# Performance work log

Hardware: AMD Instinct MI355X
Metric: run time of the kernel (lower is better)

The kernel has to match this reference:

```python
import jax, jax.numpy as jnp
import numpy as np
import math

N = 8192
NFEAT = 63
NHID = 1024
NLAYERS = 7
LAMBDA = 1.5
ALPHA = 0.7
NEG = -1e12


def setup_inputs() -> dict:
    key = jax.random.key(0)
    ks = jax.random.split(key, 12)
    x = jax.random.normal(ks[0], (N, NFEAT), dtype=jnp.float32)
    # dist acts as a (normalized) propagation matrix; scale by 1/N for numerical stability
    dist = jax.random.uniform(ks[1], (N, N), dtype=jnp.float32) / N
    adj = jax.random.randint(ks[2], (N, N), 0, 2, dtype=jnp.int32)
    # parameters
    fc_W = jax.random.normal(ks[3], (NFEAT, NHID), dtype=jnp.float32) * 0.1
    fc_b = jnp.zeros((NHID,), dtype=jnp.float32)
    stdv = 1.0 / math.sqrt(NHID)
    conv_W = jax.random.uniform(ks[4], (NLAYERS, NHID, NHID), dtype=jnp.float32,
                                minval=-stdv, maxval=stdv)
    gat_W = jax.random.normal(ks[5], (NHID, NHID), dtype=jnp.float32) * (1.414 / math.sqrt(NHID))
    gat_a = jax.random.normal(ks[6], (2 * NHID, 1), dtype=jnp.float32) * 0.05
    cls1_W = jax.random.normal(ks[7], (NHID, 64), dtype=jnp.float32) * (1.0 / math.sqrt(NHID))
    cls1_b = jnp.zeros((64,), dtype=jnp.float32)
    cls3_W = jax.random.normal(ks[8], (64, 1), dtype=jnp.float32) * 0.125
    cls3_b = jnp.zeros((1,), dtype=jnp.float32)
    return {"x": x, "dist": dist, "adj": adj, "fc_W": fc_W, "fc_b": fc_b,
            "conv_W": conv_W, "gat_W": gat_W, "gat_a": gat_a,
            "cls1_W": cls1_W, "cls1_b": cls1_b, "cls3_W": cls3_W, "cls3_b": cls3_b}


def _theta(l):
    return min(1.0, math.log(LAMBDA / l + 1.0))


def reference(x, dist, adj, fc_W, fc_b, conv_W, gat_W, gat_a, cls1_W, cls1_b, cls3_W, cls3_b):
    # eval mode: all dropouts are identity
    h = jax.nn.relu(x @ fc_W + fc_b)          # [N, H]
    h0 = h
    # GCNII-style propagation layers
    for i in range(NLAYERS):
        theta = _theta(i + 1)
        hi = dist @ h                          # [N, H] sparse-style propagation
        support = (1.0 - ALPHA) * hi + ALPHA * h0
        out = theta * (support @ conv_W[i]) + (1.0 - theta) * support + h
        h = jax.nn.relu(out)
    # GAT layer (l = 9). Faithful math, but computed without the N*N*2F tensor:
    # e_ij = leakyrelu(h_i' @ a1 + h_j' @ a2) with h' = h @ W
    hp = h @ gat_W                             # [N, H]
    a1 = gat_a[:NHID, 0]                       # [H]
    a2 = gat_a[NHID:, 0]                       # [H]
    e = jax.nn.leaky_relu(hp @ a1[:, None] + (hp @ a2[:, None]).T, negative_slope=0.2)  # [N, N]
    e = jnp.where(adj > 0, e, NEG)
    attention = jax.nn.softmax(e, axis=1)      # [N, N]
    theta = _theta(9)
    hi = attention @ h                         # note: attends over layer input h, not hp
    support = (1.0 - ALPHA) * hi + ALPHA * h0
    out = theta * (support @ gat_W) + (1.0 - theta) * support + h
    h = jax.nn.elu(out)
    h = jax.nn.relu(h @ cls1_W + cls1_b)
    out = jax.nn.sigmoid(h @ cls3_W + cls3_b)  # [N, 1]
    return out.squeeze(-1)                     # [N]
```

## Files before the change

### kernel.cpp

```cpp
#include <hip/hip_runtime.h>
#include <math.h>

#define NN 8192
#define NH 1024

typedef __bf16 bf16x8 __attribute__((ext_vector_type(8)));
typedef float floatx4 __attribute__((ext_vector_type(4)));
typedef unsigned short us8 __attribute__((ext_vector_type(8)));
typedef unsigned short us;

__device__ __forceinline__ unsigned short f2bf(float f) {
  unsigned int u = __float_as_uint(f);
  u += 0x7fffu + ((u >> 16) & 1u);
  return (unsigned short)(u >> 16);
}

__device__ __forceinline__ void async16(const void* g, void* l) {
  __builtin_amdgcn_global_load_lds(
      (__attribute__((address_space(1))) void*)(g),
      (__attribute__((address_space(3))) void*)(l), 16, 0, 0);
}

__global__ __launch_bounds__(512, 2)
void gemm_big(const us* __restrict__ A, const us* __restrict__ Bt,
              const float* __restrict__ aux, float* __restrict__ supf,
              us* __restrict__ supb)
{
  __shared__ __align__(16) us lsm[73728];
  us* lB = lsm;
  us* lA = lsm + 24576;

  const int id = blockIdx.x;
  const int yt = id & 31;
  const int xt = id >> 5;

  const int tid  = threadIdx.x;
  const int lane = tid & 63;
  const int wave = tid >> 6;
  const long tileM = (long)yt * 256;
  const long tileN = (long)xt * 128;
  const int wm = (wave & 3) * 64;
  const int wn = (wave >> 2) * 64;

  const int chunk8 = (tid & 7) ^ ((tid >> 3) & 7);
  const us* gA0 = A + (tileM + (tid >> 3)) * 8192L + chunk8 * 8;
  const us* gB0 = Bt + (tileN + (tid >> 3)) * 8192L + chunk8 * 8;
  const int lo = tid * 8;

  const int fr = lane & 15;
  const int q  = lane >> 4;
  const int cx0 = ((q) ^ (fr & 7)) * 8;
  const int cx1 = ((4 + q) ^ (fr & 7)) * 8;

  floatx4 zero4 = {0.f, 0.f, 0.f, 0.f};
  floatx4 acc[4][4];
#pragma unroll
  for (int i = 0; i < 4; ++i)
#pragma unroll
    for (int j = 0; j < 4; ++j) acc[i][j] = zero4;

#define STAGE_BIG(s, kf)                                                  \
  {                                                                       \
    const long ko = (long)(kf) << 6;                                      \
    async16(gA0 + ko,              lA + (s)*16384 + lo);                  \
    async16(gA0 + 64 * 8192L + ko, lA + (s)*16384 + 4096 + lo);           \
    async16(gA0 + 128 * 8192L + ko, lA + (s)*16384 + 8192 + lo);          \
    async16(gA0 + 192 * 8192L + ko, lA + (s)*16384 + 12288 + lo);         \
    async16(gB0 + ko,              lB + (s)*8192 + lo);                   \
    async16(gB0 + 64 * 8192L + ko, lB + (s)*8192 + 4096 + lo);            \
  }

#define KSTEP_BIG(s, kf)                                                  \
  {                                                                       \
    asm volatile("s_waitcnt vmcnt(6)\n\ts_barrier" ::: "memory");         \
    STAGE_BIG((((s) + 2) % 3), kf);                                       \
    bf16x8 af[2][4], bfr[2][4];                                           \
    _Pragma("unroll") for (int i = 0; i < 4; ++i) {                       \
      af[0][i] = *(const bf16x8*)&lA[(s)*16384 + (wm + 16 * i + fr) * 64 + cx0]; \
      af[1][i] = *(const bf16x8*)&lA[(s)*16384 + (wm + 16 * i + fr) * 64 + cx1]; \
    }                                                                     \
    _Pragma("unroll") for (int j = 0; j < 4; ++j) {                       \
      bfr[0][j] = *(const bf16x8*)&lB[(s)*8192 + (wn + 16 * j + fr) * 64 + cx0]; \
      bfr[1][j] = *(const bf16x8*)&lB[(s)*8192 + (wn + 16 * j + fr) * 64 + cx1]; \
    }                                                                     \
    _Pragma("unroll") for (int kk = 0; kk < 2; ++kk)                      \
      _Pragma("unroll") for (int i = 0; i < 4; ++i)                       \
        _Pragma("unroll") for (int j = 0; j < 4; ++j)                     \
            acc[i][j] = __builtin_amdgcn_mfma_f32_16x16x32_bf16(          \
                af[kk][i], bfr[kk][j], acc[i][j], 0, 0, 0);               \
  }

  STAGE_BIG(0, 0)
  STAGE_BIG(1, 1)

  for (int kt = 0; kt < 126; kt += 3) {
    KSTEP_BIG(0, kt + 2)
    KSTEP_BIG(1, kt + 3)
    KSTEP_BIG(2, kt + 4)
  }
  KSTEP_BIG(0, 127)
  KSTEP_BIG(1, 127)
  asm volatile("s_waitcnt vmcnt(0)" ::: "memory");

  const int crow = (lane >> 4) * 4;
#pragma unroll
  for (int i = 0; i < 4; ++i)
#pragma unroll
    for (int j = 0; j < 4; ++j)
#pragma unroll
      for (int r = 0; r < 4; ++r) {
        long row = tileM + wm + 16 * i + crow + r;
        long col = tileN + wn + 16 * j + fr;
        long idx = row * NH + col;
        float s = 0.3f * acc[i][j][r] + 0.7f * aux[idx];
        supf[idx] = s;
        supb[idx] = f2bf(s);
      }
#undef STAGE_BIG
#undef KSTEP_BIG
}

template<int EPI>
__global__ __launch_bounds__(256)
void gemm_db(const us* __restrict__ A, const us* __restrict__ Bt, int K,
             const float* __restrict__ aux, float* __restrict__ iof,
             us* __restrict__ outb, us* __restrict__ hTb, float theta)
{
  __shared__ __align__(16) us lsm[32768];
  us* lB = lsm;
  us* lA = lsm + 16384;

  const int id = blockIdx.x;
  const int xcd = id & 7, slot = id >> 3;
  const int xt = slot & 7;
  const int yt = xcd + 8 * (slot >> 3);

  const int tid  = threadIdx.x;
  const int lane = tid & 63;
  const int wave = tid >> 6;
  const long tileM = (long)yt * 128;
  const long tileN = (long)xt * 128;
  const int wm = (wave & 1) * 64;
  const int wn = (wave >> 1) * 64;

  const int chunk = (tid & 3) ^ ((tid >> 3) & 3);
  const us* gA0 = A + (tileM + (tid >> 2)) * (long)K + chunk * 8;
  const us* gA1 = gA0 + 64L * K;
  const us* gB0 = Bt + (tileN + (tid >> 2)) * (long)K + chunk * 8;
  const us* gB1 = gB0 + 64L * K;
  const int lo = tid * 8;

  const int fr = lane & 15;
  const int q8 = (lane >> 4) * 8;
  const int q8x = q8 ^ ((fr & 6) << 2);

  floatx4 zero4 = {0.f, 0.f, 0.f, 0.f};
  floatx4 acc[4][4];
#pragma unroll
  for (int i = 0; i < 4; ++i)
#pragma unroll
    for (int j = 0; j < 4; ++j) acc[i][j] = zero4;

#define STAGE_DB(s, kf)                                                   \
  {                                                                       \
    const int k0 = (kf) << 5;                                             \
    async16(gA0 + k0, lA + (s)*4096 + lo);                                \
    async16(gA1 + k0, lA + (s)*4096 + 2048 + lo);                         \
    async16(gB0 + k0, lB + (s)*4096 + lo);                                \
    async16(gB1 + k0, lB + (s)*4096 + 2048 + lo);                         \
  }

#define KSTEP_DB(s, kf)                                                   \
  {                                                                       \
    asm volatile("s_waitcnt vmcnt(8)\n\ts_barrier" ::: "memory");         \
    STAGE_DB((((s) + 3) & 3), kf);                                        \
    bf16x8 af[4], bfr[4];                                                 \
    _Pragma("unroll") for (int i = 0; i < 4; ++i)                         \
        af[i] = *(const bf16x8*)&lA[(s)*4096 + (wm + 16 * i + fr) * 32 + q8x]; \
    _Pragma("unroll") for (int j = 0; j < 4; ++j)                         \
        bfr[j] = *(const bf16x8*)&lB[(s)*4096 + (wn + 16 * j + fr) * 32 + q8x]; \
    _Pragma("unroll") for (int i = 0; i < 4; ++i)                         \
        _Pragma("unroll") for (int j = 0; j < 4; ++j)                     \
            acc[i][j] = __builtin_amdgcn_mfma_f32_16x16x32_bf16(          \
                af[i], bfr[j], acc[i][j], 0, 0, 0);                       \
  }

  STAGE_DB(0, 0)
  STAGE_DB(1, 1)
  STAGE_DB(2, 2)

  for (int kt = 0; kt < 32; kt += 4) {
    int k3 = kt + 3; if (k3 > 31) k3 = 31;
    int k4 = kt + 4; if (k4 > 31) k4 = 31;
    int k5 = kt + 5; if (k5 > 31) k5 = 31;
    int k6 = kt + 6; if (k6 > 31) k6 = 31;
    KSTEP_DB(0, k3)
    KSTEP_DB(1, k4)
    KSTEP_DB(2, k5)
    KSTEP_DB(3, k6)
  }
  asm volatile("s_waitcnt vmcnt(0)" ::: "memory");
  __syncthreads();

  us* ldsT = lsm;
  const int crow = (lane >> 4) * 4;
#pragma unroll
  for (int i = 0; i < 4; ++i) {
#pragma unroll
    for (int j = 0; j < 4; ++j) {
#pragma unroll
      for (int r = 0; r < 4; ++r) {
        int lr = wm + 16 * i + crow + r;
        int lc = wn + 16 * j + fr;
        long idx = (tileM + lr) * NH + tileN + lc;
        float o = theta * acc[i][j][r] + (1.f - theta) * aux[idx] + iof[idx];
        o = (EPI == 1) ? fmaxf(o, 0.f) : (o > 0.f ? o : __expf(o) - 1.f);
        iof[idx] = o;
        if (EPI == 1) ldsT[lc * 136 + lr] = f2bf(o);
        if (EPI == 2) outb[idx] = f2bf(o);
      }
    }
  }
  if (EPI == 1) {
    __syncthreads();
    int c = tid >> 1, half = tid & 1;
#pragma unroll
    for (int it = 0; it < 8; ++it) {
      int r = half * 64 + it * 8;
      us8 v = *(const us8*)&ldsT[c * 136 + r];
      *(us8*)&hTb[(tileN + c) * 8192L + tileM + r] = v;
    }
  }
#undef STAGE_DB
#undef KSTEP_DB
}

__global__ __launch_bounds__(256)
void cls_gemm(const us* __restrict__ hb, const us* __restrict__ W1t,
              const float* __restrict__ b1, const float* __restrict__ W3,
              const float* __restrict__ b3, float* __restrict__ out)
{
  __shared__ __align__(16) us lA[4096];
  __shared__ __align__(16) us lB[2048];
  const int tid = threadIdx.x, lane = tid & 63, wave = tid >> 6;
  const long tileM = (long)blockIdx.x * 128;
  const us* gA0 = hb + (tileM + (tid >> 2)) * 1024L + (tid & 3) * 8;
  const us* gA1 = gA0 + 64 * 1024L;
  const us* gB0 = W1t + (tid >> 2) * 1024L + (tid & 3) * 8;
  const int fr = lane & 15, q8 = (lane >> 4) * 8;
  const int wm = wave * 32;

  floatx4 zero4 = {0.f, 0.f, 0.f, 0.f};
  floatx4 acc[2][4];
#pragma unroll
  for (int i = 0; i < 2; ++i)
#pragma unroll
    for (int j = 0; j < 4; ++j) acc[i][j] = zero4;

  for (int kt = 0; kt < 32; ++kt) {
    const int k0 = kt << 5;
    async16(gA0 + k0, lA + tid * 8);
    async16(gA1 + k0, lA + 2048 + tid * 8);
    async16(gB0 + k0, lB + tid * 8);
    __syncthreads();
    bf16x8 af[2], bfr[4];
#pragma unroll
    for (int i = 0; i < 2; ++i)
      af[i] = *(const bf16x8*)&lA[(wm + 16 * i + fr) * 32 + q8];
#pragma unroll
    for (int j = 0; j < 4; ++j)
      bfr[j] = *(const bf16x8*)&lB[(16 * j + fr) * 32 + q8];
#pragma unroll
    for (int i = 0; i < 2; ++i)
#pragma unroll
      for (int j = 0; j < 4; ++j)
        acc[i][j] = __builtin_amdgcn_mfma_f32_16x16x32_bf16(af[i], bfr[j], acc[i][j], 0, 0, 0);
    __syncthreads();
  }

  float b1v[4], w3v[4];
#pragma unroll
  for (int j = 0; j < 4; ++j) { b1v[j] = b1[16 * j + fr]; w3v[j] = W3[16 * j + fr]; }
  const float b3v = b3[0];
  const int crow = (lane >> 4) * 4;
#pragma unroll
  for (int i = 0; i < 2; ++i)
#pragma unroll
    for (int r = 0; r < 4; ++r) {
      float v = 0.f;
#pragma unroll
      for (int j = 0; j < 4; ++j)
        v += fmaxf(acc[i][j][r] + b1v[j], 0.f) * w3v[j];
      v += __shfl_xor(v, 1);
      v += __shfl_xor(v, 2);
      v += __shfl_xor(v, 4);
      v += __shfl_xor(v, 8);
      if (fr == 0)
        out[tileM + wm + 16 * i + crow + r] = 1.f / (1.f + __expf(-(v + b3v)));
    }
}

__global__ __launch_bounds__(256)
void transpose_f32_bf16(const float* __restrict__ src, us* __restrict__ dst,
                        int R, int C) {
  __shared__ float t[32][33];
  int tid = threadIdx.x;
  int tx = tid & 31, ty = tid >> 5;
  long r0 = (long)blockIdx.y * 32, c0 = (long)blockIdx.x * 32;
#pragma unroll
  for (int i = 0; i < 32; i += 8)
    t[ty + i][tx] = src[(r0 + ty + i) * C + c0 + tx];
  __syncthreads();
#pragma unroll
  for (int i = 0; i < 32; i += 8)
    dst[(c0 + ty + i) * R + r0 + tx] = f2bf(t[tx][ty + i]);
}

__global__ __launch_bounds__(256)
void f32_to_bf16_vec(const float* __restrict__ s, us* __restrict__ d) {
  long i = (blockIdx.x * 256L + threadIdx.x) * 4;
  float4 v = *(const float4*)(s + i);
  *(ushort4*)(d + i) = make_ushort4(f2bf(v.x), f2bf(v.y), f2bf(v.z), f2bf(v.w));
}

__global__ __launch_bounds__(256)
void fc_kernel(const float* __restrict__ x, const float* __restrict__ W,
               const float* __restrict__ b, float* __restrict__ h0f,
               float* __restrict__ hf) {
  __shared__ float xs[64];
  int row = blockIdx.x, tid = threadIdx.x;
  if (tid < 63) xs[tid] = x[row * 63 + tid];
  __syncthreads();
#pragma unroll
  for (int q = 0; q < 4; ++q) {
    int c = tid + q * 256;
    float s = b[c];
    for (int k = 0; k < 63; ++k) s += xs[k] * W[k * NH + c];
    s = fmaxf(s, 0.f);
    long idx = (long)row * NH + c;
    h0f[idx] = s;
    hf[idx] = s;
  }
}

__global__ __launch_bounds__(256)
void wv_kernel(const float* __restrict__ W, const float* __restrict__ a,
               float* __restrict__ va1, float* __restrict__ va2) {
  int k = blockIdx.x, tid = threadIdx.x;
  float s1 = 0.f, s2 = 0.f;
  for (int n = tid; n < NH; n += 256) {
    float w = W[(long)k * NH + n];
    s1 += w * a[n];
    s2 += w * a[NH + n];
  }
#pragma unroll
  for (int o = 32; o; o >>= 1) { s1 += __shfl_down(s1, o); s2 += __shfl_down(s2, o); }
  __shared__ float r1[4], r2[4];
  int wave = tid >> 6;
  if ((tid & 63) == 0) { r1[wave] = s1; r2[wave] = s2; }
  __syncthreads();
  if (tid == 0) {
    va1[k] = r1[0] + r1[1] + r1[2] + r1[3];
    va2[k] = r2[0] + r2[1] + r2[2] + r2[3];
  }
}

__global__ __launch_bounds__(256)
void fg_kernel(const float* __restrict__ h, const float* __restrict__ va1,
               const float* __restrict__ va2, float* __restrict__ fv,
               float* __restrict__ gv) {
  int row = blockIdx.x, tid = threadIdx.x;
  float s1 = 0.f, s2 = 0.f;
  for (int k = tid; k < NH; k += 256) {
    float v = h[(long)row * NH + k];
    s1 += v * va1[k];
    s2 += v * va2[k];
  }
#pragma unroll
  for (int o = 32; o; o >>= 1) { s1 += __shfl_down(s1, o); s2 += __shfl_down(s2, o); }
  __shared__ float r1[4], r2[4];
  int wave = tid >> 6;
  if ((tid & 63) == 0) { r1[wave] = s1; r2[wave] = s2; }
  __syncthreads();
  if (tid == 0) {
    fv[row] = r1[0] + r1[1] + r1[2] + r1[3];
    gv[row] = r2[0] + r2[1] + r2[2] + r2[3];
  }
}

__global__ __launch_bounds__(256)
void attn_ml(const int* __restrict__ adj, const float* __restrict__ f,
             const float* __restrict__ g, float* __restrict__ Mr,
             float* __restrict__ Lr) {
  const int row = blockIdx.x, tid = threadIdx.x;
  const float fi = f[row];
  const int4* arow = (const int4*)(adj + (long)row * NN);
  float m = -3.0e38f, s = 0.f;
  for (int c = tid; c < NN / 4; c += 256) {
    int4 a = arow[c];
    float4 gg = *(const float4*)(g + c * 4);
#pragma unroll
    for (int t = 0; t < 4; ++t) {
      int av = (t == 0) ? a.x : (t == 1) ? a.y : (t == 2) ? a.z : a.w;
      float gvv = (t == 0) ? gg.x : (t == 1) ? gg.y : (t == 2) ? gg.z : gg.w;
      if (av > 0) {
        float e = fi + gvv;
        e = e > 0.f ? e : 0.2f * e;
        if (e > m) { s = s * __expf(m - e) + 1.f; m = e; }
        else s += __expf(e - m);
      }
    }
  }
#pragma unroll
  for (int o = 32; o; o >>= 1) {
    float m2 = __shfl_down(m, o), s2 = __shfl_down(s, o);
    float mn = fmaxf(m, m2);
    s = s * __expf(m - mn) + s2 * __expf(m2 - mn);
    m = mn;
  }
  __shared__ float ms[4], ss[4];
  int wave = tid >> 6;
  if ((tid & 63) == 0) { ms[wave] = m; ss[wave] = s; }
  __syncthreads();
  if (tid == 0) {
    float mm = ms[0], sv = ss[0];
    for (int w = 1; w < 4; ++w) {
      float mn = fmaxf(mm, ms[w]);
      sv = sv * __expf(mm - mn) + ss[w] * __expf(ms[w] - mn);
      mm = mn;
    }
    Mr[row] = mm;
    Lr[row] = sv;
  }
}

__global__ __launch_bounds__(256)
void attn_p(const int* __restrict__ adj, const float* __restrict__ f,
            const float* __restrict__ g, const float* __restrict__ Mr,
            const float* __restrict__ Lr, us* __restrict__ P) {
  long gid = blockIdx.x * 256L + threadIdx.x;
  int row = (int)(gid >> 11);
  int jc = (int)(gid & 2047) * 4;
  float fi = f[row], m = Mr[row], l = Lr[row];
  bool uni = !(l > 0.f);
  float inv = uni ? 0.f : 1.f / l;
  int4 a = *(const int4*)(adj + ((long)row << 13) + jc);
  float4 gg = *(const float4*)(g + jc);
  float p[4];
#pragma unroll
  for (int t = 0; t < 4; ++t) {
    int av = (t == 0) ? a.x : (t == 1) ? a.y : (t == 2) ? a.z : a.w;
    float gvv = (t == 0) ? gg.x : (t == 1) ? gg.y : (t == 2) ? gg.z : gg.w;
    float e = fi + gvv;
    e = e > 0.f ? e : 0.2f * e;
    float pv = (av > 0) ? __expf(e - m) * inv : 0.f;
    if (uni) pv = 1.f / (float)NN;
    p[t] = pv;
  }
  *(ushort4*)(P + ((long)row << 13) + jc) =
      make_ushort4(f2bf(p[0]), f2bf(p[1]), f2bf(p[2]), f2bf(p[3]));
}

extern "C" void kernel_launch(void* const* d_in, const int* in_sizes, int n_in,
                              void* d_out, int out_size, void* d_ws, size_t ws_size,
                              hipStream_t stream) {
  const float* x      = (const float*)d_in[0];
  const float* dist   = (const float*)d_in[1];
  const int*   adj    = (const int*)d_in[2];
  const float* fc_W   = (const float*)d_in[3];
  const float* fc_b   = (const float*)d_in[4];
  const float* conv_W = (const float*)d_in[5];
  const float* gat_W  = (const float*)d_in[6];
  const float* gat_a  = (const float*)d_in[7];
  const float* cls1_W = (const float*)d_in[8];
  const float* cls1_b = (const float*)d_in[9];
  const float* cls3_W = (const float*)d_in[10];
  const float* cls3_b = (const float*)d_in[11];
  float* out = (float*)d_out;

  char* p = (char*)d_ws;
  auto alloc = [&](size_t bytes) {
    char* r = p;
    p += (bytes + 255) & ~(size_t)255;
    return r;
  };
  us* distb   = (us*)alloc((size_t)NN * NN * 2);
  float* h0f  = (float*)alloc((size_t)NN * NH * 4);
  float* hf   = (float*)alloc((size_t)NN * NH * 4);
  float* supf = (float*)alloc((size_t)NN * NH * 4);
  us* supb    = (us*)alloc((size_t)NN * NH * 2);
  us* hb      = (us*)alloc((size_t)NN * NH * 2);
  us* hTb     = (us*)alloc((size_t)NN * NH * 2);
  us* convWT  = (us*)alloc((size_t)7 * NH * NH * 2);
  us* gatWT   = (us*)alloc((size_t)NH * NH * 2);
  us* W1t     = (us*)alloc((size_t)64 * NH * 2);
  float* va1 = (float*)alloc(NH * 4);
  float* va2 = (float*)alloc(NH * 4);
  float* fv  = (float*)alloc(NN * 4);
  float* gv  = (float*)alloc(NN * 4);
  float* Mr  = (float*)alloc(NN * 4);
  float* Lr  = (float*)alloc(NN * 4);

  float th[7];
  for (int l = 0; l < 7; ++l) {
    float t = logf(1.5f / (float)(l + 1) + 1.f);
    th[l] = t < 1.f ? t : 1.f;
  }
  float th9 = logf(1.5f / 9.f + 1.f);

  f32_to_bf16_vec<<<(NN * (long)NN) / (4 * 256), 256, 0, stream>>>(dist, distb);
  for (int i = 0; i < 7; ++i)
    transpose_f32_bf16<<<dim3(32, 32), 256, 0, stream>>>(
        conv_W + (size_t)i * NH * NH, convWT + (size_t)i * NH * NH, NH, NH);
  transpose_f32_bf16<<<dim3(32, 32), 256, 0, stream>>>(gat_W, gatWT, NH, NH);
  transpose_f32_bf16<<<dim3(2, 32), 256, 0, stream>>>(cls1_W, W1t, NH, 64);

  fc_kernel<<<NN, 256, 0, stream>>>(x, fc_W, fc_b, h0f, hf);
  transpose_f32_bf16<<<dim3(NH / 32, NN / 32), 256, 0, stream>>>(hf, hTb, NN, NH);

  for (int l = 0; l < 7; ++l) {
    gemm_big<<<256, 512, 0, stream>>>(distb, hTb, h0f, supf, supb);
    gemm_db<1><<<512, 256, 0, stream>>>(supb, convWT + (size_t)l * NH * NH, NH,
                                        supf, hf, nullptr, hTb, th[l]);
  }

  wv_kernel<<<NH, 256, 0, stream>>>(gat_W, gat_a, va1, va2);
  fg_kernel<<<NN, 256, 0, stream>>>(hf, va1, va2, fv, gv);
  attn_ml<<<NN, 256, 0, stream>>>(adj, fv, gv, Mr, Lr);
  attn_p<<<(NN * (long)NN) / (4 * 256), 256, 0, stream>>>(adj, fv, gv, Mr, Lr, distb);

  gemm_big<<<256, 512, 0, stream>>>(distb, hTb, h0f, supf, supb);
  gemm_db<2><<<512, 256, 0, stream>>>(supb, gatWT, NH, supf, hf, hb, nullptr, th9);

  cls_gemm<<<64, 256, 0, stream>>>(hb, W1t, cls1_b, cls3_W, cls3_b, out);
}
```

Before: 2.190 ms.

## Fuse attention softmax stats and probability write into one kernel; coalesce transpose stores

Merges the row max/sum kernel and the probability-writing kernel into a single per-row kernel, so the adj row is re-read while it is likely still in cache instead of in a separate pass, and the Mr/Lr buffers and one launch are removed. It also remaps the transposed hTb store in the gemm_db epilogue so that 16 consecutive threads write one contiguous 256-byte segment of a column row, which should coalesce better. The fused kernel writes P row by row with 256 threads per row, which may give less parallelism per row than the old flat grid.

```diff
diff --git a/kernel.cpp b/kernel.cpp
--- a/kernel.cpp
+++ b/kernel.cpp
@@ -167,7 +167,7 @@
     async16(gA0 + k0, lA + (s)*4096 + lo);                                \
     async16(gA1 + k0, lA + (s)*4096 + 2048 + lo);                         \
     async16(gB0 + k0, lB + (s)*4096 + lo);                                \
-    async16(gB1 + k0, lB + (s)*4096 + 2048 + lo);                         \
+    async16(gB1 + k0, lB + (s)*4096 + 2048 + lo);                        \
   }
 
 #define KSTEP_DB(s, kf)                                                   \
@@ -223,12 +223,13 @@
   }
   if (EPI == 1) {
     __syncthreads();
-    int c = tid >> 1, half = tid & 1;
+    int ch = tid & 15;
+    int c0 = tid >> 4;
 #pragma unroll
     for (int it = 0; it < 8; ++it) {
-      int r = half * 64 + it * 8;
-      us8 v = *(const us8*)&ldsT[c * 136 + r];
-      *(us8*)&hTb[(tileN + c) * 8192L + tileM + r] = v;
+      int c = c0 + it * 16;
+      us8 v = *(const us8*)&ldsT[c * 136 + ch * 8];
+      *(us8*)&hTb[(tileN + c) * 8192L + tileM + ch * 8] = v;
     }
   }
 #undef STAGE_DB
@@ -389,9 +390,8 @@
 }
 
 __global__ __launch_bounds__(256)
-void attn_ml(const int* __restrict__ adj, const float* __restrict__ f,
-             const float* __restrict__ g, float* __restrict__ Mr,
-             float* __restrict__ Lr) {
+void attn_fused(const int* __restrict__ adj, const float* __restrict__ f,
+                const float* __restrict__ g, us* __restrict__ P) {
   const int row = blockIdx.x, tid = threadIdx.x;
   const float fi = f[row];
   const int4* arow = (const int4*)(adj + (long)row * NN);
@@ -418,7 +418,7 @@
     s = s * __expf(m - mn) + s2 * __expf(m2 - mn);
     m = mn;
   }
-  __shared__ float ms[4], ss[4];
+  __shared__ float ms[4], ss[4], bcast[2];
   int wave = tid >> 6;
   if ((tid & 63) == 0) { ms[wave] = m; ss[wave] = s; }
   __syncthreads();
@@ -429,36 +429,30 @@
       sv = sv * __expf(mm - mn) + ss[w] * __expf(ms[w] - mn);
       mm = mn;
     }
-    Mr[row] = mm;
-    Lr[row] = sv;
-  }
-}
-
-__global__ __launch_bounds__(256)
-void attn_p(const int* __restrict__ adj, const float* __restrict__ f,
-            const float* __restrict__ g, const float* __restrict__ Mr,
-            const float* __restrict__ Lr, us* __restrict__ P) {
-  long gid = blockIdx.x * 256L + threadIdx.x;
-  int row = (int)(gid >> 11);
-  int jc = (int)(gid & 2047) * 4;
-  float fi = f[row], m = Mr[row], l = Lr[row];
-  bool uni = !(l > 0.f);
-  float inv = uni ? 0.f : 1.f / l;
-  int4 a = *(const int4*)(adj + ((long)row << 13) + jc);
-  float4 gg = *(const float4*)(g + jc);
-  float p[4];
-#pragma unroll
-  for (int t = 0; t < 4; ++t) {
-    int av = (t == 0) ? a.x : (t == 1) ? a.y : (t == 2) ? a.z : a.w;
-    float gvv = (t == 0) ? gg.x : (t == 1) ? gg.y : (t == 2) ? gg.z : gg.w;
-    float e = fi + gvv;
-    e = e > 0.f ? e : 0.2f * e;
-    float pv = (av > 0) ? __expf(e - m) * inv : 0.f;
-    if (uni) pv = 1.f / (float)NN;
-    p[t] = pv;
-  }
-  *(ushort4*)(P + ((long)row << 13) + jc) =
-      make_ushort4(f2bf(p[0]), f2bf(p[1]), f2bf(p[2]), f2bf(p[3]));
+    bcast[0] = mm;
+    bcast[1] = sv;
+  }
+  __syncthreads();
+  const float M = bcast[0], L = bcast[1];
+  const bool uni = !(L > 0.f);
+  const float inv = uni ? 0.f : 1.f / L;
+  for (int c = tid; c < NN / 4; c += 256) {
+    int4 a = arow[c];
+    float4 gg = *(const float4*)(g + c * 4);
+    float p[4];
+#pragma unroll
+    for (int t = 0; t < 4; ++t) {
+      int av = (t == 0) ? a.x : (t == 1) ? a.y : (t == 2) ? a.z : a.w;
+      float gvv = (t == 0) ? gg.x : (t == 1) ? gg.y : (t == 2) ? gg.z : gg.w;
+      float e = fi + gvv;
+      e = e > 0.f ? e : 0.2f * e;
+      float pv = (av > 0) ? __expf(e - M) * inv : 0.f;
+      if (uni) pv = 1.f / (float)NN;
+      p[t] = pv;
+    }
+    *(ushort4*)(P + ((long)row << 13) + c * 4) =
+        make_ushort4(f2bf(p[0]), f2bf(p[1]), f2bf(p[2]), f2bf(p[3]));
+  }
 }
 
 extern "C" void kernel_launch(void* const* d_in, const int* in_sizes, int n_in,
@@ -498,8 +492,6 @@
   float* va2 = (float*)alloc(NH * 4);
   float* fv  = (float*)alloc(NN * 4);
   float* gv  = (float*)alloc(NN * 4);
-  float* Mr  = (float*)alloc(NN * 4);
-  float* Lr  = (float*)alloc(NN * 4);
 
   float th[7];
   for (int l = 0; l < 7; ++l) {
@@ -526,8 +518,7 @@
 
   wv_kernel<<<NH, 256, 0, stream>>>(gat_W, gat_a, va1, va2);
   fg_kernel<<<NN, 256, 0, stream>>>(hf, va1, va2, fv, gv);
-  attn_ml<<<NN, 256, 0, stream>>>(adj, fv, gv, Mr, Lr);
-  attn_p<<<(NN * (long)NN) / (4 * 256), 256, 0, stream>>>(adj, fv, gv, Mr, Lr, distb);
+  attn_fused<<<NN, 256, 0, stream>>>(adj, fv, gv, distb);
 
   gemm_big<<<256, 512, 0, stream>>>(distb, hTb, h0f, supf, supb);
   gemm_db<2><<<512, 256, 0, stream>>>(supb, gatWT, NH, supf, hf, hb, nullptr, th9);
```

Result: no change. 2.178 ms (-0.6%).
